# Optimization experiments

Hardware: AMD Instinct MI355X
Metric: run time of the kernel (lower is better)

The kernel has to match this reference:

```python
import jax, jax.numpy as jnp
import numpy as np

G = 128        # grid resolution per axis (points are voxel centers on this grid)
N = 262144     # number of input points == number of output points
CIN = 16
COUT = 32


def _build_neighbors(inp_coords, out_coords):
    """Emulates FixedRadiusSearch(Linf, r=1.53*voxel) + invert_neighbors_list on a
    unit grid: for each output point and each of the 27 kernel taps t, find the
    (unique) input point at out_coord - (t-1), or -1 if that voxel is empty."""
    enc = lambda c: (c[:, 0].astype(np.int64) * G + c[:, 1]) * G + c[:, 2]
    inp_keys = enc(inp_coords)
    order = np.argsort(inp_keys)
    skeys = inp_keys[order]
    nbr = np.full((out_coords.shape[0], 27), -1, dtype=np.int32)
    k = 0
    for t0 in range(3):
        for t1 in range(3):
            for t2 in range(3):
                d = np.array([t0 - 1, t1 - 1, t2 - 1], dtype=np.int64)
                nc = out_coords - d  # input voxel s.t. (out - inp) == d
                valid = np.all((nc >= 0) & (nc < G), axis=1)
                keys = enc(np.clip(nc, 0, G - 1))
                pos = np.searchsorted(skeys, keys).clip(0, len(skeys) - 1)
                found = valid & (skeys[pos] == keys)
                nbr[:, k] = np.where(found, order[pos].astype(np.int32), -1)
                k += 1
    return nbr


def setup_inputs() -> dict:
    rng = np.random.default_rng(0)
    # unique voxels -> at most one point per voxel (regular-grid assumption)
    inp_keys = rng.choice(G ** 3, size=N, replace=False)
    out_keys = rng.choice(G ** 3, size=N, replace=False)
    dec = lambda kk: np.stack([kk // (G * G), (kk // G) % G, kk % G], axis=1).astype(np.int64)
    nbr_idx = jnp.asarray(_build_neighbors(dec(inp_keys), dec(out_keys)))

    key = jax.random.key(0)
    k1, k2 = jax.random.split(key)
    inp_features = jax.random.normal(k1, (N, CIN), dtype=jnp.float32)
    # matches kernel_initializer = uniform_(-0.05, 0.05)
    kernel = jax.random.uniform(k2, (3, 3, 3, CIN, COUT), dtype=jnp.float32,
                                minval=-0.05, maxval=0.05)
    bias = jnp.zeros((COUT,), dtype=jnp.float32)  # bias_initializer = zeros_
    return {"inp_features": inp_features, "kernel": kernel, "bias": bias,
            "nbr_idx": nbr_idx}


def reference(inp_features, kernel, bias, nbr_idx):
    # continuous_conv_transpose with interpolation='nearest_neighbor',
    # coordinate_mapping='identity', normalize=False on a unit grid:
    # out[j] = sum_t W[t] @ f[nbr(j, t)]  (missing taps contribute zero), + bias
    valid = (nbr_idx >= 0)
    idx = jnp.where(valid, nbr_idx, 0)
    gathered = inp_features[idx] * valid[..., None].astype(inp_features.dtype)  # [N,27,Cin]
    W = kernel.reshape(27, kernel.shape[-2], kernel.shape[-1])                  # [27,Cin,Cout]
    return jnp.einsum('nkc,kco->no', gathered, W) + bias
```

## Files before the change

kernel.cpp:

```cpp
#include <hip/hip_runtime.h>
#include <hip/hip_bf16.h>

#define NPTS  262144
#define CIN   16
#define COUT  32
#define NTAPS 27
#define BLK   256
#define DEPTH 8

#define WIMG_SHORTS (NTAPS * 512)
#define WIMG_PAD    14336
#define FEATB_OFF   28672

typedef __attribute__((ext_vector_type(8)))  short short8v;
typedef __attribute__((ext_vector_type(16))) float f32x16;

__global__ __launch_bounds__(256) void prep_kernel(
    const float* __restrict__ feat, const float* __restrict__ Wg,
    short* __restrict__ wimg, __hip_bfloat16* __restrict__ fb)
{
    if (blockIdx.x < NPTS * CIN / 4 / 256) {
        const int i = blockIdx.x * 256 + threadIdx.x;
        const float4 x = ((const float4*)feat)[i];
        __hip_bfloat162* o = (__hip_bfloat162*)(fb + CIN);
        o[2 * i]     = __float22bfloat162_rn(float2{x.x, x.y});
        o[2 * i + 1] = __float22bfloat162_rn(float2{x.z, x.w});
    } else {
        for (int i = threadIdx.x; i < WIMG_PAD; i += 256) {
            short v = 0;
            if (i < WIMG_SHORTS) {
                const int tap  = i >> 9;
                const int r    = i & 511;
                const int ln   = r >> 3;
                const int e    = r & 7;
                const int cin  = ((ln >> 5) << 3) + e;
                const int cout = ln & 31;
                const __hip_bfloat16 h =
                    __float2bfloat16(Wg[(tap * CIN + cin) * COUT + cout]);
                v = *(const short*)&h;
            }
            wimg[i] = v;
        }
        if (threadIdx.x < 2)
            ((int4*)fb)[threadIdx.x] = int4{0, 0, 0, 0};
    }
}

template<bool USE_WS>
__global__ __launch_bounds__(BLK, 4) void sct_mfma_kernel(
    const float* __restrict__ feat,
    const __hip_bfloat16* __restrict__ featb,
    const short* __restrict__ wimg,
    const float* __restrict__ Wg,
    const float* __restrict__ bias,
    const int*   __restrict__ nbr,
    float*       __restrict__ out)
{
    __shared__ short bpack[WIMG_PAD];

    const int tid = threadIdx.x;
    if (USE_WS) {
        #pragma unroll
        for (int q = 0; q < 7; ++q) {
            const int off = q * (256 * 8) + tid * 8;
            *(short8v*)&bpack[off] = *(const short8v*)&wimg[off];
        }
    } else {
        for (int i = tid; i < WIMG_SHORTS; i += BLK) {
            const int tap  = i >> 9;
            const int r    = i & 511;
            const int ln   = r >> 3;
            const int e    = r & 7;
            const int cin  = ((ln >> 5) << 3) + e;
            const int cout = ln & 31;
            const __hip_bfloat16 h =
                __float2bfloat16(Wg[(tap * CIN + cin) * COUT + cout]);
            bpack[i] = *(const short*)&h;
        }
    }
    __syncthreads();

    const int lane = tid & 63;
    const int wv   = tid >> 6;
    const int p0   = blockIdx.x * 128 + wv * 32;
    const int prow = lane & 31;
    const int g    = lane >> 5;
    const int* nb  = nbr + (long)(p0 + prow) * NTAPS;

    int nid[NTAPS];
    #pragma unroll
    for (int q = 0; q < 6; ++q) {
        const int4 v = *(const int4*)(nb + 4 * q);
        nid[4*q+0] = v.x; nid[4*q+1] = v.y; nid[4*q+2] = v.z; nid[4*q+3] = v.w;
    }
    {
        const int2 v2 = *(const int2*)(nb + 24);
        nid[24] = v2.x; nid[25] = v2.y; nid[26] = nb[26];
    }

    f32x16 acc;
    {
        const float b = bias[prow];
        #pragma unroll
        for (int r2 = 0; r2 < 16; ++r2) acc[r2] = b;
    }

    short8v af[DEPTH];
    const __hip_bfloat16* fshift = featb + CIN;

    auto gather1 = [&](int t, short8v& dst) {
        if (USE_WS) {
            dst = *(const short8v*)(fshift + (long)nid[t] * CIN + g * 8);
        } else {
            const int id = nid[t];
            short8v a = {};
            if (id >= 0) {
                const float4* fp = (const float4*)(feat + (long)id * CIN + g * 8);
                const float4 x = fp[0];
                const float4 y = fp[1];
                union { short8v v; __hip_bfloat162 h[4]; } u;
                u.h[0] = __float22bfloat162_rn(float2{x.x, x.y});
                u.h[1] = __float22bfloat162_rn(float2{x.z, x.w});
                u.h[2] = __float22bfloat162_rn(float2{y.x, y.y});
                u.h[3] = __float22bfloat162_rn(float2{y.z, y.w});
                a = u.v;
            }
            dst = a;
        }
    };

    #pragma unroll
    for (int t = 0; t < DEPTH; ++t) gather1(t, af[t]);

    #pragma unroll
    for (int t = 0; t < NTAPS; ++t) {
        const short8v bf = *(const short8v*)&bpack[(t << 9) + (lane << 3)];
        acc = __builtin_amdgcn_mfma_f32_32x32x16_bf16(af[t % DEPTH], bf, acc, 0, 0, 0);
        if (t + DEPTH < NTAPS) gather1(t + DEPTH, af[(t + DEPTH) % DEPTH]);
    }

    #pragma unroll
    for (int r2 = 0; r2 < 16; ++r2) {
        const int row = (r2 & 3) + 8 * (r2 >> 2) + 4 * g;
        out[(long)(p0 + row) * COUT + prow] = acc[r2];
    }
}

extern "C" void kernel_launch(void* const* d_in, const int* in_sizes, int n_in,
                              void* d_out, int out_size, void* d_ws, size_t ws_size,
                              hipStream_t stream) {
    const float* feat = (const float*)d_in[0];
    const float* Wg   = (const float*)d_in[1];
    const float* bias = (const float*)d_in[2];
    const int*   nbr  = (const int*)d_in[3];
    float*       out  = (float*)d_out;

    const size_t need = FEATB_OFF + (size_t)(NPTS + 1) * CIN * sizeof(__hip_bfloat16);
    if (ws_size >= need) {
        short* wimg = (short*)d_ws;
        __hip_bfloat16* fb = (__hip_bfloat16*)((char*)d_ws + FEATB_OFF);
        prep_kernel<<<NPTS * CIN / 4 / 256 + 1, 256, 0, stream>>>(feat, Wg, wimg, fb);
        sct_mfma_kernel<true><<<NPTS / 128, BLK, 0, stream>>>(
            feat, fb, wimg, Wg, bias, nbr, out);
    } else {
        sct_mfma_kernel<false><<<NPTS / 128, BLK, 0, stream>>>(
            feat, nullptr, nullptr, Wg, bias, nbr, out);
    }
}
```

Before: 47.92 us.

## Stream neighbor feature gathers into LDS via global_load_lds with explicit vmcnt pipeline

Replaces register-held gathered feature fragments with direct global-to-LDS DMA loads into per-wave ring slots, six deep. Explicit s_waitcnt vmcnt values and sched barriers control how many gathers stay in flight while each MFMA consumes a slot. The aim is to cut register pressure and keep the gathers in flight, but it adds LDS traffic and LDS footprint, and launch bounds drop occupancy from 4 to 3 blocks per CU. The 16-byte global_load_lds size needs gfx950-class support.

```diff
diff --git a/kernel.cpp b/kernel.cpp
--- a/kernel.cpp
+++ b/kernel.cpp
@@ -6,7 +6,8 @@
 #define COUT  32
 #define NTAPS 27
 #define BLK   256
-#define DEPTH 8
+#define NWAVE 4
+#define DEPTH 6
 
 #define WIMG_SHORTS (NTAPS * 512)
 #define WIMG_PAD    14336
@@ -14,6 +15,8 @@
 
 typedef __attribute__((ext_vector_type(8)))  short short8v;
 typedef __attribute__((ext_vector_type(16))) float f32x16;
+
+#define VMCNT(N) asm volatile("s_waitcnt vmcnt(" #N ")" ::: "memory")
 
 __global__ __launch_bounds__(256) void prep_kernel(
     const float* __restrict__ feat, const float* __restrict__ Wg,
@@ -47,7 +50,7 @@
 }
 
 template<bool USE_WS>
-__global__ __launch_bounds__(BLK, 4) void sct_mfma_kernel(
+__global__ __launch_bounds__(BLK, 3) void sct_mfma_kernel(
     const float* __restrict__ feat,
     const __hip_bfloat16* __restrict__ featb,
     const short* __restrict__ wimg,
@@ -57,6 +60,7 @@
     float*       __restrict__ out)
 {
     __shared__ short bpack[WIMG_PAD];
+    __shared__ __align__(16) short aslot[NWAVE][DEPTH][512];
 
     const int tid = threadIdx.x;
     if (USE_WS) {
@@ -105,13 +109,42 @@
         for (int r2 = 0; r2 < 16; ++r2) acc[r2] = b;
     }
 
-    short8v af[DEPTH];
-    const __hip_bfloat16* fshift = featb + CIN;
+    if (USE_WS) {
+        const __hip_bfloat16* fshift = featb + CIN;
+        const int elo = g * 8;
 
-    auto gather1 = [&](int t, short8v& dst) {
-        if (USE_WS) {
-            dst = *(const short8v*)(fshift + (long)nid[t] * CIN + g * 8);
-        } else {
+        auto dma = [&](int t) {
+            const __hip_bfloat16* ga = fshift + (long)nid[t] * CIN + elo;
+            __builtin_amdgcn_global_load_lds((const void*)ga,
+                                             (void*)&aslot[wv][t % DEPTH][0],
+                                             16, 0, 0);
+        };
+
+        VMCNT(0);
+        #pragma unroll
+        for (int t = 0; t < DEPTH; ++t) dma(t);
+
+        #pragma unroll
+        for (int t = 0; t < NTAPS; ++t) {
+            const int rem = NTAPS - 1 - t;
+            if (rem >= 5)      VMCNT(5);
+            else if (rem == 4) VMCNT(4);
+            else if (rem == 3) VMCNT(3);
+            else if (rem == 2) VMCNT(2);
+            else if (rem == 1) VMCNT(1);
+            else               VMCNT(0);
+            __builtin_amdgcn_sched_barrier(0);
+            const short8v af = *(const short8v*)&aslot[wv][t % DEPTH][lane << 3];
+            const short8v bf = *(const short8v*)&bpack[(t << 9) + (lane << 3)];
+            acc = __builtin_amdgcn_mfma_f32_32x32x16_bf16(af, bf, acc, 0, 0, 0);
+            if (t + DEPTH < NTAPS) {
+                __builtin_amdgcn_sched_barrier(0);
+                dma(t + DEPTH);
+            }
+        }
+    } else {
+        #pragma unroll
+        for (int t = 0; t < NTAPS; ++t) {
             const int id = nid[t];
             short8v a = {};
             if (id >= 0) {
@@ -125,18 +158,9 @@
                 u.h[3] = __float22bfloat162_rn(float2{y.z, y.w});
                 a = u.v;
             }
-            dst = a;
+            const short8v bf = *(const short8v*)&bpack[(t << 9) + (lane << 3)];
+            acc = __builtin_amdgcn_mfma_f32_32x32x16_bf16(a, bf, acc, 0, 0, 0);
         }
-    };
-
-    #pragma unroll
-    for (int t = 0; t < DEPTH; ++t) gather1(t, af[t]);
-
-    #pragma unroll
-    for (int t = 0; t < NTAPS; ++t) {
-        const short8v bf = *(const short8v*)&bpack[(t << 9) + (lane << 3)];
-        acc = __builtin_amdgcn_mfma_f32_32x32x16_bf16(af[t % DEPTH], bf, acc, 0, 0, 0);
-        if (t + DEPTH < NTAPS) gather1(t + DEPTH, af[(t + DEPTH) % DEPTH]);
     }
 
     #pragma unroll
```

Measured after the change: 59.52 us. 24.2% more time.
